# Kernel tuning notes

Hardware: AMD Instinct MI355X
Metric: run time of the kernel (lower is better)

Reference implementation:

```python
import jax, jax.numpy as jnp
import numpy as np

B, S = 256, 500
NQ, DQ, DV, M, F = 10000, 128, 256, 50, 512


def _kaiming(key, shape, fan_in):
    return jax.random.normal(key, shape, dtype=jnp.float32) * np.sqrt(2.0 / fan_in)


def setup_inputs() -> dict:
    key = jax.random.key(0)
    ks = jax.random.split(key, 24)
    inp = {
        'q_data': jax.random.randint(ks[0], (B, S), 0, NQ, dtype=jnp.int32),
        'qa_data': jax.random.randint(ks[1], (B, S), 0, 2 * NQ, dtype=jnp.int32),
        'target': jax.random.randint(ks[2], (B, S), 0, 3, dtype=jnp.int32),
        'time_data': jax.random.randint(ks[3], (B, S), 0, 9902, dtype=jnp.int32),
        'attempt_data': jax.random.randint(ks[4], (B, S), 0, 4000, dtype=jnp.int32),
        'hint_data': jax.random.randint(ks[5], (B, S), 0, 60, dtype=jnp.int32),
        'hintTotal_data': jax.random.randint(ks[6], (B, S), 0, 60, dtype=jnp.int32),
    }
    # embedding tables (padding row 0 zeroed, as in torch padding_idx=0)
    inp['q_emb'] = _kaiming(ks[7], (NQ + 1, DQ), DQ).at[0].set(0.0)
    inp['qa_emb'] = _kaiming(ks[8], (2 * NQ + 1, DV), DV).at[0].set(0.0)
    inp['time_emb'] = _kaiming(ks[9], (9902, DQ), DQ).at[0].set(0.0)
    inp['attempt_emb'] = _kaiming(ks[10], (4000, DQ), DQ).at[0].set(0.0)
    inp['hint_total_emb'] = _kaiming(ks[11], (60, DQ), DQ).at[0].set(0.0)
    # memory init
    inp['Mk'] = _kaiming(ks[12], (M, DQ), DQ)
    inp['Mv0'] = _kaiming(ks[13], (M, DV), DV)
    # difficulty linears (shared weights applied twice)
    inp['diff_W'] = _kaiming(ks[14], (DQ, DQ), DQ)
    inp['diff_b'] = jnp.zeros((DQ,), jnp.float32)
    inp['diff2_W'] = _kaiming(ks[15], (DQ, DQ), DQ)
    inp['diff2_b'] = jnp.zeros((DQ,), jnp.float32)
    # DKVMN write head: erase/add linears (DV -> DV)
    inp['erase_W'] = _kaiming(ks[16], (DV, DV), DV)
    inp['erase_b'] = jnp.zeros((DV,), jnp.float32)
    inp['add_W'] = _kaiming(ks[17], (DV, DV), DV)
    inp['add_b'] = jnp.zeros((DV,), jnp.float32)
    # readout
    inp['read_W'] = _kaiming(ks[18], (F, DV + DQ), DV + DQ)
    inp['read_b'] = jnp.zeros((F,), jnp.float32)
    inp['pred_W'] = _kaiming(ks[19], (1, F), F)
    inp['pred_b'] = jnp.zeros((1,), jnp.float32)
    return inp


def reference(q_data, qa_data, target, time_data, attempt_data, hint_data, hintTotal_data,
              q_emb, qa_emb, time_emb, attempt_emb, hint_total_emb,
              Mk, Mv0, diff_W, diff_b, diff2_W, diff2_b,
              erase_W, erase_b, add_W, add_b, read_W, read_b, pred_W, pred_b):
    lin1 = lambda x: x @ diff_W.T + diff_b
    lin2 = lambda x: x @ diff2_W.T + diff2_b

    qe = q_emb[q_data]                        # [B,S,DQ]
    te = time_emb[time_data]
    ae = attempt_emb[attempt_data]
    he = hint_total_emb[hint_data]            # forward uses hint_total_embed for both
    hte = hint_total_emb[hintTotal_data]

    time_final = jax.nn.sigmoid(lin2(jnp.tanh(lin1(te + qe))))
    diff_final = jax.nn.sigmoid(lin2(jnp.tanh(lin1(hte + he + ae + qe))))
    q_proc = lin1(qe + diff_final * (he + hte + ae))  # [B,S,DQ]
    qa_e = qa_emb[qa_data]                            # [B,S,DV]

    Mv_init = jnp.broadcast_to(Mv0[None], (q_data.shape[0], M, DV))

    def step(Mv, inp):
        q, qa = inp                                   # [B,DQ], [B,DV]
        w = jax.nn.softmax(q @ Mk.T, axis=-1)         # [B,M]
        read = jnp.einsum('bm,bmd->bd', w, Mv)        # [B,DV]
        e = jax.nn.sigmoid(qa @ erase_W.T + erase_b)  # [B,DV]
        a = jnp.tanh(qa @ add_W.T + add_b)            # [B,DV]
        Mv = Mv * (1.0 - w[:, :, None] * e[:, None, :]) + w[:, :, None] * a[:, None, :]
        return Mv, read

    _, reads = jax.lax.scan(step, Mv_init,
                            (jnp.swapaxes(q_proc, 0, 1), jnp.swapaxes(qa_e, 0, 1)))
    reads = jnp.swapaxes(reads, 0, 1)                 # [B,S,DV]

    input_embed = q_proc + time_final * te            # [B,S,DQ]
    predict_input = jnp.concatenate([reads, input_embed], axis=-1)
    rc = jnp.tanh(predict_input @ read_W.T + read_b)  # [B,S,F]
    pred = (rc @ pred_W.T + pred_b).reshape(-1)       # [B*S]

    t1 = target.reshape(-1)
    mask = t1 >= 1
    y = jnp.where(mask, t1 - 1, 0).astype(jnp.float32)
    # BCE with logits: log(1+e^x) - x*y
    lelem = jnp.logaddexp(0.0, pred) - pred * y
    n = jnp.maximum(jnp.sum(mask.astype(jnp.float32)), 1.0)
    loss = jnp.sum(jnp.where(mask, lelem, 0.0)) / n
    maskf = mask.astype(jnp.float32)
    return loss, jax.nn.sigmoid(pred) * maskf, y * maskf
```

## Files before the change

kernel.cpp:

```cpp
#include <hip/hip_runtime.h>
#include <cstdint>
#include <cstddef>

#define NB 256
#define SQ 500
#define NROWS (NB * SQ)
#define DQ 128
#define DV 256
#define MM 50
#define FF 512
#define NQA 20096
#define WSTRIDE 52
#define WT 10

typedef _Float16 half8 __attribute__((ext_vector_type(8)));
typedef float floatx4 __attribute__((ext_vector_type(4)));
typedef float f2 __attribute__((ext_vector_type(2)));
typedef unsigned int u32;
typedef unsigned short u16;

typedef __attribute__((address_space(1))) void gvoid;
typedef __attribute__((address_space(3))) void lvoid;

__device__ __forceinline__ void gl16(const u16* g, u16* l) {
    __builtin_amdgcn_global_load_lds((gvoid*)g, (lvoid*)l, 16, 0, 0);
}

__device__ __forceinline__ float4 ld4(const float* p) {
    return *reinterpret_cast<const float4*>(p);
}
__device__ __forceinline__ float sigf(float x) { return 1.f / (1.f + __expf(-x)); }
__device__ __forceinline__ float tanhfast(float x) { return 2.f / (1.f + __expf(-2.f * x)) - 1.f; }
__device__ __forceinline__ int gmap(int l, int s0, int CS) {
    int b = (unsigned)l / (unsigned)CS;
    return b * SQ + s0 + (l - b * CS);
}
__device__ __forceinline__ void st4h(u16* dst, float4 v) {
    _Float16 h0 = (_Float16)v.x, h1 = (_Float16)v.y, h2 = (_Float16)v.z, h3 = (_Float16)v.w;
    ushort4 u;
    u.x = *(u16*)&h0; u.y = *(u16*)&h1; u.z = *(u16*)&h2; u.w = *(u16*)&h3;
    *(ushort4*)dst = u;
}
__device__ __forceinline__ float h2f(u16 b) { _Float16 h; *(u16*)&h = b; return (float)h; }
__device__ __forceinline__ u16 f2h(float x) { _Float16 h = (_Float16)x; return *(u16*)&h; }

__global__ __launch_bounds__(256) void cvt16(
    const float* __restrict__ s, u16* __restrict__ d, int n4)
{
    int i = blockIdx.x * 256 + threadIdx.x;
    if (i < n4) st4h(d + 4 * (size_t)i, ld4(s + 4 * (size_t)i));
}

__global__ __launch_bounds__(256) void wcvt(
    const float* __restrict__ s0, const float* __restrict__ s1,
    const float* __restrict__ s2, const float* __restrict__ s3,
    const float* __restrict__ s4, u16* __restrict__ dst)
{
    int i = blockIdx.x * 256 + threadIdx.x;
    if (i >= 90112) return;
    const float* s; int off;
    if (i < 4096)       { s = s0; off = 0; }
    else if (i < 8192)  { s = s1; off = 4096; }
    else if (i < 24576) { s = s2; off = 8192; }
    else if (i < 40960) { s = s3; off = 24576; }
    else                { s = s4; off = 40960; }
    st4h(dst + 4 * (size_t)i, ld4(s + 4 * (size_t)(i - off)));
}

__global__ __launch_bounds__(256) void mkcvt(
    const float* __restrict__ Mk, u16* __restrict__ Mkh)
{
    int i = blockIdx.x * 256 + threadIdx.x;
    if (i >= 64 * 32) return;
    int row = i >> 5;
    float4 v = (row < MM) ? ld4(Mk + (size_t)row * DQ + (i & 31) * 4)
                          : float4{0.f, 0.f, 0.f, 0.f};
    st4h(Mkh + 4 * (size_t)i, v);
}

__global__ __launch_bounds__(256) void prep128(
    const int* __restrict__ q_data, const int* __restrict__ time_data,
    const int* __restrict__ attempt_data, const int* __restrict__ hint_data,
    const int* __restrict__ hintT_data,
    const float* __restrict__ q_emb, const float* __restrict__ time_emb,
    const float* __restrict__ attempt_emb, const float* __restrict__ ht_emb,
    u16* __restrict__ Xp, u16* __restrict__ S3p, u16* __restrict__ QEp,
    int s0, int CS, int Nc)
{
    int g = blockIdx.x * 256 + threadIdx.x;
    int l = g >> 5;
    int kq = (g & 31) << 2;
    if (l >= Nc) return;
    int n = gmap(l, s0, CS);
    float4 qe  = ld4(q_emb       + (size_t)q_data[n]       * DQ + kq);
    float4 te  = ld4(time_emb    + (size_t)time_data[n]    * DQ + kq);
    float4 ae  = ld4(attempt_emb + (size_t)attempt_data[n] * DQ + kq);
    float4 he  = ld4(ht_emb      + (size_t)hint_data[n]    * DQ + kq);
    float4 hte = ld4(ht_emb      + (size_t)hintT_data[n]   * DQ + kq);
    size_t off = (size_t)l * DQ + kq;
    float4 x1, s3, x2;
    x1.x = te.x + qe.x; x1.y = te.y + qe.y; x1.z = te.z + qe.z; x1.w = te.w + qe.w;
    s3.x = he.x + hte.x + ae.x; s3.y = he.y + hte.y + ae.y;
    s3.z = he.z + hte.z + ae.z; s3.w = he.w + hte.w + ae.w;
    x2.x = s3.x + qe.x; x2.y = s3.y + qe.y; x2.z = s3.z + qe.z; x2.w = s3.w + qe.w;
    st4h(Xp + off, x1);
    st4h(Xp + (size_t)Nc * DQ + off, x2);
    st4h(S3p + off, s3);
    st4h(QEp + off, qe);
}

__global__ __launch_bounds__(256, 2) void gemm12(
    const u16* __restrict__ A, const u16* __restrict__ W1h,
    const u16* __restrict__ W2h, const float* __restrict__ b1,
    const float* __restrict__ b2, u16* __restrict__ Yh,
    const u16* __restrict__ QEp, const u16* __restrict__ S3p, int Nc)
{
    __shared__ u16 smem[32768];
    u16* At = smem;
    u16* Bt = smem + 8192;
    u16* Tt = smem + 16384;
    const int tid = threadIdx.x;
    const int row0 = blockIdx.x * 128;
    const int lane = tid & 63, wv = tid >> 6;
    const int wr = (wv >> 1) * 64, wc = (wv & 1) * 64;
    const int q = lane >> 4, c0 = lane & 15;

    floatx4 acc[4][4];
#pragma unroll
    for (int m = 0; m < 4; ++m)
#pragma unroll
        for (int n = 0; n < 4; ++n) acc[m][n] = (floatx4)0.f;

    for (int kt = 0; kt < 128; kt += 64) {
#pragma unroll
        for (int j = 0; j < 4; ++j) {
            int f = tid + j * 256; int r = f >> 3; int lg = (f & 7) ^ (r & 7);
            gl16(A + (size_t)(row0 + r) * 128 + kt + lg * 8, &At[f * 8]);
        }
#pragma unroll
        for (int j = 0; j < 4; ++j) {
            int f = tid + j * 256; int r = f >> 3; int lg = (f & 7) ^ (r & 7);
            gl16(W1h + (size_t)r * 128 + kt + lg * 8, &Bt[f * 8]);
        }
        __syncthreads();
#pragma unroll
        for (int kk = 0; kk < 2; ++kk) {
            half8 af[4], bf[4];
#pragma unroll
            for (int m = 0; m < 4; ++m) {
                int row = wr + m * 16 + c0;
                af[m] = *(half8*)&At[row * 64 + ((((kk << 2) | q)) ^ (row & 7)) * 8];
            }
#pragma unroll
            for (int n = 0; n < 4; ++n) {
                int row = wc + n * 16 + c0;
                bf[n] = *(half8*)&Bt[row * 64 + ((((kk << 2) | q)) ^ (row & 7)) * 8];
            }
#pragma unroll
            for (int m = 0; m < 4; ++m)
#pragma unroll
                for (int n = 0; n < 4; ++n)
                    acc[m][n] = __builtin_amdgcn_mfma_f32_16x16x32_f16(af[m], bf[n], acc[m][n], 0, 0, 0);
        }
        __syncthreads();
    }

    {
        float bv1[4];
#pragma unroll
        for (int n = 0; n < 4; ++n) bv1[n] = b1[wc + n * 16 + c0];
#pragma unroll
        for (int m = 0; m < 4; ++m)
#pragma unroll
            for (int r4 = 0; r4 < 4; ++r4) {
                int row = wr + m * 16 + q * 4 + r4;
#pragma unroll
                for (int n = 0; n < 4; ++n) {
                    int col = wc + n * 16 + c0;
                    float v = tanhfast(acc[m][n][r4] + bv1[n]);
                    int tile = col >> 6, cl = col & 63, gl = cl >> 3;
                    Tt[tile * 8192 + row * 64 + ((gl ^ (row & 7)) << 3) + (cl & 7)] = f2h(v);
                }
            }
    }
#pragma unroll
    for (int m = 0; m < 4; ++m)
#pragma unroll
        for (int n = 0; n < 4; ++n) acc[m][n] = (floatx4)0.f;

#pragma unroll
    for (int j = 0; j < 4; ++j) {
        int f = tid + j * 256; int r = f >> 3; int lg = (f & 7) ^ (r & 7);
        gl16(W2h + (size_t)r * 128 + 0 + lg * 8, &Bt[f * 8]);
    }
    __syncthreads();

#pragma unroll
    for (int kt = 0; kt < 2; ++kt) {
#pragma unroll
        for (int kk = 0; kk < 2; ++kk) {
            half8 af[4], bf[4];
#pragma unroll
            for (int m = 0; m < 4; ++m) {
                int row = wr + m * 16 + c0;
                af[m] = *(half8*)&Tt[kt * 8192 + row * 64 + ((((kk << 2) | q)) ^ (row & 7)) * 8];
            }
#pragma unroll
            for (int n = 0; n < 4; ++n) {
                int row = wc + n * 16 + c0;
                bf[n] = *(half8*)&Bt[row * 64 + ((((kk << 2) | q)) ^ (row & 7)) * 8];
            }
#pragma unroll
            for (int m = 0; m < 4; ++m)
#pragma unroll
                for (int n = 0; n < 4; ++n)
                    acc[m][n] = __builtin_amdgcn_mfma_f32_16x16x32_f16(af[m], bf[n], acc[m][n], 0, 0, 0);
        }
        if (kt == 0) {
            __syncthreads();
#pragma unroll
            for (int j = 0; j < 4; ++j) {
                int f = tid + j * 256; int r = f >> 3; int lg = (f & 7) ^ (r & 7);
                gl16(W2h + (size_t)r * 128 + 64 + lg * 8, &Bt[f * 8]);
            }
            __syncthreads();
        }
    }

    float bv[4];
#pragma unroll
    for (int n = 0; n < 4; ++n) bv[n] = b2[wc + n * 16 + c0];
#pragma unroll
    for (int m = 0; m < 4; ++m)
#pragma unroll
        for (int r4 = 0; r4 < 4; ++r4) {
            int row = row0 + wr + m * 16 + q * 4 + r4;
#pragma unroll
            for (int n = 0; n < 4; ++n) {
                int col = wc + n * 16 + c0;
                float v = sigf(acc[m][n][r4] + bv[n]);
                if (row < Nc) {
                    Yh[(size_t)row * 128 + col] = f2h(v);
                } else {
                    size_t o = (size_t)(row - Nc) * 128 + col;
                    float qe = h2f(QEp[o]), s3 = h2f(S3p[o]);
                    Yh[(size_t)row * 128 + col] = f2h(fmaf(v, s3, qe));
                }
            }
        }
}

__global__ __launch_bounds__(256, 2) void gemm3w(
    const u16* __restrict__ X3, const u16* __restrict__ W1h,
    const float* __restrict__ b1, const u16* __restrict__ Mkh,
    const int* __restrict__ tidx, const float* __restrict__ temb,
    const u16* __restrict__ TF, u16* __restrict__ RDIE,
    float* __restrict__ Wb, int s0, int CS)
{
    __shared__ u16 smem[32768];
    u16* At = smem;
    u16* Bt = smem + 8192;
    u16* Tt = smem + 16384;
    const int tid = threadIdx.x;
    const int row0 = blockIdx.x * 128;
    const int lane = tid & 63, wv = tid >> 6;
    const int wr = (wv >> 1) * 64, wc = (wv & 1) * 64;
    const int q = lane >> 4, c0 = lane & 15;

    floatx4 acc[4][4];
#pragma unroll
    for (int m = 0; m < 4; ++m)
#pragma unroll
        for (int n = 0; n < 4; ++n) acc[m][n] = (floatx4)0.f;

    for (int kt = 0; kt < 128; kt += 64) {
#pragma unroll
        for (int j = 0; j < 4; ++j) {
            int f = tid + j * 256; int r = f >> 3; int lg = (f & 7) ^ (r & 7);
            gl16(X3 + (size_t)(row0 + r) * 128 + kt + lg * 8, &At[f * 8]);
        }
#pragma unroll
        for (int j = 0; j < 4; ++j) {
            int f = tid + j * 256; int r = f >> 3; int lg = (f & 7) ^ (r & 7);
            gl16(W1h + (size_t)r * 128 + kt + lg * 8, &Bt[f * 8]);
        }
        __syncthreads();
#pragma unroll
        for (int kk = 0; kk < 2; ++kk) {
            half8 af[4], bf[4];
#pragma unroll
            for (int m = 0; m < 4; ++m) {
                int row = wr + m * 16 + c0;
                af[m] = *(half8*)&At[row * 64 + ((((kk << 2) | q)) ^ (row & 7)) * 8];
            }
#pragma unroll
            for (int n = 0; n < 4; ++n) {
                int row = wc + n * 16 + c0;
                bf[n] = *(half8*)&Bt[row * 64 + ((((kk << 2) | q)) ^ (row & 7)) * 8];
            }
#pragma unroll
            for (int m = 0; m < 4; ++m)
#pragma unroll
                for (int n = 0; n < 4; ++n)
                    acc[m][n] = __builtin_amdgcn_mfma_f32_16x16x32_f16(af[m], bf[n], acc[m][n], 0, 0, 0);
        }
        __syncthreads();
    }

    {
        float bv1[4];
#pragma unroll
        for (int n = 0; n < 4; ++n) bv1[n] = b1[wc + n * 16 + c0];
#pragma unroll
        for (int m = 0; m < 4; ++m)
#pragma unroll
            for (int r4 = 0; r4 < 4; ++r4) {
                int rloc = wr + m * 16 + q * 4 + r4;
                int grow = row0 + rloc;
                int nmap = gmap(grow, s0, CS);
                const float* terow = temb + (size_t)tidx[nmap] * 128;
#pragma unroll
                for (int n = 0; n < 4; ++n) {
                    int col = wc + n * 16 + c0;
                    float qp = acc[m][n][r4] + bv1[n];
                    int tile = col >> 6, cl = col & 63, gl = cl >> 3;
                    Tt[tile * 8192 + rloc * 64 + ((gl ^ (rloc & 7)) << 3) + (cl & 7)] = f2h(qp);
                    float tf = h2f(TF[(size_t)grow * 128 + col]);
                    RDIE[(size_t)grow * 384 + 256 + col] = f2h(fmaf(tf, terow[col], qp));
                }
            }
    }
#pragma unroll
    for (int j = 0; j < 4; ++j) {
        int f = tid + j * 256;
        int fl = f & 511;
        int ktile = f >> 9;
        int r = fl >> 3;
        int lg = (fl & 7) ^ (r & 7);
        gl16(Mkh + (size_t)r * 128 + ktile * 64 + lg * 8, &Bt[f * 8]);
    }
    __syncthreads();

    const int wrW = wv * 32;
    floatx4 acc2[2][4];
#pragma unroll
    for (int m = 0; m < 2; ++m)
#pragma unroll
        for (int n = 0; n < 4; ++n) acc2[m][n] = (floatx4)0.f;
#pragma unroll
    for (int kt = 0; kt < 2; ++kt)
#pragma unroll
        for (int kk = 0; kk < 2; ++kk) {
            half8 af[2], bf[4];
#pragma unroll
            for (int m = 0; m < 2; ++m) {
                int row = wrW + m * 16 + c0;
                af[m] = *(half8*)&Tt[kt * 8192 + row * 64 + ((((kk << 2) | q)) ^ (row & 7)) * 8];
            }
#pragma unroll
            for (int n = 0; n < 4; ++n) {
                int row = n * 16 + c0;
                bf[n] = *(half8*)&Bt[kt * 4096 + row * 64 + ((((kk << 2) | q)) ^ (row & 7)) * 8];
            }
#pragma unroll
            for (int m = 0; m < 2; ++m)
#pragma unroll
                for (int n = 0; n < 4; ++n)
                    acc2[m][n] = __builtin_amdgcn_mfma_f32_16x16x32_f16(af[m], bf[n], acc2[m][n], 0, 0, 0);
        }
    __syncthreads();

    float* Sred = (float*)smem;
#pragma unroll
    for (int m = 0; m < 2; ++m)
#pragma unroll
        for (int r4 = 0; r4 < 4; ++r4) {
            int row = wrW + m * 16 + q * 4 + r4;
#pragma unroll
            for (int n = 0; n < 4; ++n)
                Sred[row * 67 + n * 16 + c0] = acc2[m][n][r4];
        }
    __syncthreads();

    if (tid < 128) {
        float* s = &Sred[tid * 67];
        float mx = -3.0e38f;
#pragma unroll
        for (int m = 0; m < MM; ++m) mx = fmaxf(mx, s[m]);
        float sum = 0.f;
#pragma unroll
        for (int m = 0; m < MM; ++m) { float e = __expf(s[m] - mx); s[m] = e; sum += e; }
        float inv = 1.f / sum;
#pragma unroll
        for (int m = 0; m < MM; ++m) s[m] *= inv;
        s[50] = 0.f; s[51] = 0.f;
    }
    __syncthreads();

    for (int i = tid; i < 128 * 13; i += 256) {
        int row = i / 13, seg = i - row * 13;
        float4 v;
        v.x = Sred[row * 67 + seg * 4 + 0];
        v.y = Sred[row * 67 + seg * 4 + 1];
        v.z = Sred[row * 67 + seg * 4 + 2];
        v.w = Sred[row * 67 + seg * 4 + 3];
        *(float4*)(Wb + (size_t)(row0 + row) * WSTRIDE + seg * 4) = v;
    }
}

template <int MODE>
__global__ __launch_bounds__(256, 2) void gemm16(
    const u16* __restrict__ A, const u16* __restrict__ W0,
    const u16* __restrict__ W1, const float* __restrict__ b0,
    const float* __restrict__ b1, u16* __restrict__ Yh,
    float* __restrict__ Yf,
    u16* __restrict__ AUX, const float* __restrict__ predW,
    int K)
{
    __shared__ u16 smem[2 * 128 * 64];
    u16* At = smem;
    u16* Bt = smem + 128 * 64;
    const int tid = threadIdx.x;
    const int row0 = blockIdx.x * 128;
    const int by = blockIdx.y;

    const u16* Wp;
    int col0;
    if constexpr (MODE == 4) { Wp = (by < 2) ? W0 : W1; col0 = (by & 1) * 128; }
    else { Wp = W0; col0 = by * 128; }
    const float* bias = (MODE == 4 && by >= 2) ? b1 : b0;

    floatx4 acc[4][4];
#pragma unroll
    for (int m = 0; m < 4; ++m)
#pragma unroll
        for (int n = 0; n < 4; ++n) acc[m][n] = (floatx4)0.f;

    const int lane = tid & 63, wv = tid >> 6;
    const int wr = (wv >> 1) * 64, wc = (wv & 1) * 64;
    const int q = lane >> 4, c0 = lane & 15;

    for (int kt = 0; kt < K; kt += 64) {
#pragma unroll
        for (int j = 0; j < 4; ++j) {
            int f = tid + j * 256;
            int r = f >> 3;
            int lg = (f & 7) ^ (r & 7);
            gl16(A + (size_t)(row0 + r) * K + kt + lg * 8, &At[f * 8]);
        }
#pragma unroll
        for (int j = 0; j < 4; ++j) {
            int f = tid + j * 256;
            int r = f >> 3;
            int lg = (f & 7) ^ (r & 7);
            gl16(Wp + (size_t)(col0 + r) * K + kt + lg * 8, &Bt[f * 8]);
        }
        __syncthreads();
#pragma unroll
        for (int kk = 0; kk < 2; ++kk) {
            half8 af[4], bf[4];
#pragma unroll
            for (int m = 0; m < 4; ++m) {
                int row = wr + m * 16 + c0;
                af[m] = *(half8*)&At[row * 64 + ((((kk << 2) | q)) ^ (row & 7)) * 8];
            }
#pragma unroll
            for (int n = 0; n < 4; ++n) {
                int row = wc + n * 16 + c0;
                bf[n] = *(half8*)&Bt[row * 64 + ((((kk << 2) | q)) ^ (row & 7)) * 8];
            }
#pragma unroll
            for (int m = 0; m < 4; ++m)
#pragma unroll
                for (int n = 0; n < 4; ++n)
                    acc[m][n] = __builtin_amdgcn_mfma_f32_16x16x32_f16(af[m], bf[n], acc[m][n], 0, 0, 0);
        }
        __syncthreads();
    }

    float bv[4];
#pragma unroll
    for (int n = 0; n < 4; ++n) bv[n] = bias[col0 + wc + n * 16 + c0];

    if constexpr (MODE == 5) {
        float pw[4];
#pragma unroll
        for (int n = 0; n < 4; ++n) pw[n] = predW[col0 + wc + n * 16 + c0];
        float* red = (float*)smem;
#pragma unroll
        for (int m = 0; m < 4; ++m)
#pragma unroll
            for (int r4 = 0; r4 < 4; ++r4) {
                int row = wr + m * 16 + q * 4 + r4;
                float pp = 0.f;
#pragma unroll
                for (int n = 0; n < 4; ++n)
                    pp = fmaf(tanhfast(acc[m][n][r4] + bv[n]), pw[n], pp);
                red[row * 33 + (wv & 1) * 16 + c0] = pp;
            }
        __syncthreads();
        if (tid < 128) {
            float s = 0.f;
#pragma unroll
            for (int j = 0; j < 32; ++j) s += red[tid * 33 + j];
            atomicAdd(&Yf[row0 + tid], s);
        }
    } else {
#pragma unroll
        for (int m = 0; m < 4; ++m)
#pragma unroll
            for (int r4 = 0; r4 < 4; ++r4) {
                int row = row0 + wr + m * 16 + q * 4 + r4;
#pragma unroll
                for (int n = 0; n < 4; ++n) {
                    int col = col0 + wc + n * 16 + c0;
                    float v = acc[m][n][r4] + bv[n];
                    bool isE = (by < 2);
                    v = isE ? sigf(v) : tanhfast(v);
                    AUX[((size_t)row * 256 + col) * 2 + (isE ? 0 : 1)] = f2h(v);
                }
            }
    }
}

__global__ __launch_bounds__(256, 1) void scan_kernel(
    const float* __restrict__ Wb, const int* __restrict__ qa_data,
    const u32* __restrict__ EAtab,
    const float* __restrict__ Mv0, float* __restrict__ MvSt,
    u16* __restrict__ RDIE, int CS, int s0, int first)
{
    __shared__ float wt[2][WT * WSTRIDE];
    const int b = blockIdx.x;
    const int d = threadIdx.x;

    f2 mv[25];
    if (first) {
#pragma unroll
        for (int j = 0; j < 25; ++j) {
            mv[j].x = Mv0[(2 * j) * DV + d];
            mv[j].y = Mv0[(2 * j + 1) * DV + d];
        }
    } else {
#pragma unroll
        for (int j = 0; j < 25; ++j) {
            mv[j].x = MvSt[((size_t)b * MM + 2 * j) * DV + d];
            mv[j].y = MvSt[((size_t)b * MM + 2 * j + 1) * DV + d];
        }
    }

    const float* wbase = Wb + (size_t)b * CS * WSTRIDE;
    const int* qap = qa_data + (size_t)b * SQ + s0;
    u16* rp = RDIE + (size_t)b * CS * 384 + d;

    const int NT = CS / WT;
    const bool loader = (d < (WT * WSTRIDE / 4));

    if (loader) *(float4*)&wt[0][d * 4] = ld4(wbase + d * 4);
    u32 ea[WT];
    {
        int qi[WT];
#pragma unroll
        for (int i = 0; i < WT; ++i) qi[i] = qap[i];
#pragma unroll
        for (int i = 0; i < WT; ++i) ea[i] = EAtab[(size_t)qi[i] * DV + d];
    }
    __syncthreads();

    int cur = 0;
    for (int tile = 0; tile < NT; ++tile) {
        float4 wreg;
        u32 ean[WT];
        const bool havenext = (tile + 1 < NT);
        if (havenext) {
            if (loader) wreg = ld4(wbase + (size_t)(tile + 1) * WT * WSTRIDE + d * 4);
            int qn[WT];
#pragma unroll
            for (int i = 0; i < WT; ++i) qn[i] = qap[(tile + 1) * WT + i];
#pragma unroll
            for (int i = 0; i < WT; ++i) ean[i] = EAtab[(size_t)qn[i] * DV + d];
        }

        float4 wpp[2][13];
#pragma unroll
        for (int i = 0; i < 13; ++i)
            wpp[0][i] = *(const float4*)&wt[cur][i * 4];

#pragma unroll
        for (int s = 0; s < WT; ++s) {
            if (s + 1 < WT) {
#pragma unroll
                for (int i = 0; i < 13; ++i)
                    wpp[(s + 1) & 1][i] =
                        *(const float4*)&wt[cur][(s + 1) * WSTRIDE + i * 4];
            }
            const f2* w2 = (const f2*)wpp[s & 1];
            u32 eav = ea[s];
            float e = h2f((u16)(eav & 0xffff));
            float a = h2f((u16)(eav >> 16));
            f2 e2; e2.x = e; e2.y = e;
            f2 a2; a2.x = a; a2.y = a;
            f2 r0 = (f2)0.f, r1 = (f2)0.f, r2 = (f2)0.f, r3 = (f2)0.f;
#pragma unroll
            for (int j = 0; j < 24; j += 4) {
                f2 w_0 = w2[j + 0], w_1 = w2[j + 1], w_2 = w2[j + 2], w_3 = w2[j + 3];
                r0 += w_0 * mv[j + 0];
                r1 += w_1 * mv[j + 1];
                r2 += w_2 * mv[j + 2];
                r3 += w_3 * mv[j + 3];
                f2 t0 = a2 - e2 * mv[j + 0];
                f2 t1 = a2 - e2 * mv[j + 1];
                f2 t2 = a2 - e2 * mv[j + 2];
                f2 t3 = a2 - e2 * mv[j + 3];
                mv[j + 0] += w_0 * t0;
                mv[j + 1] += w_1 * t1;
                mv[j + 2] += w_2 * t2;
                mv[j + 3] += w_3 * t3;
            }
            {
                f2 w24 = w2[24];
                r0 += w24 * mv[24];
                f2 t = a2 - e2 * mv[24];
                mv[24] += w24 * t;
            }
            f2 rs = (r0 + r1) + (r2 + r3);
            rp[(size_t)(tile * WT + s) * 384] = f2h(rs.x + rs.y);
        }

        if (havenext) {
            if (loader) *(float4*)&wt[1 - cur][d * 4] = wreg;
#pragma unroll
            for (int i = 0; i < WT; ++i) ea[i] = ean[i];
            __syncthreads();
            cur ^= 1;
        }
    }

#pragma unroll
    for (int j = 0; j < 25; ++j) {
        MvSt[((size_t)b * MM + 2 * j) * DV + d]     = mv[j].x;
        MvSt[((size_t)b * MM + 2 * j + 1) * DV + d] = mv[j].y;
    }
}

__global__ __launch_bounds__(256) void loss_part(
    const float* __restrict__ P, const int* __restrict__ target,
    const float* __restrict__ pred_b, float* __restrict__ out,
    float* __restrict__ R2, int s0, int CS, int Nc)
{
    int l = blockIdx.x * 256 + threadIdx.x;
    float le = 0.f, mf = 0.f;
    if (l < Nc) {
        int n = gmap(l, s0, CS);
        float p = P[l] + pred_b[0];
        int t = target[n];
        float y = (t >= 1) ? (float)(t - 1) : 0.f;
        float sig = 1.f / (1.f + __expf(-p));
        if (t >= 1) {
            mf = 1.f;
            le = fmaxf(p, 0.f) + log1pf(__expf(-fabsf(p))) - p * y;
        }
        out[1 + n] = sig * mf;
        out[1 + NROWS + n] = y * mf;
    }
#pragma unroll
    for (int off = 32; off; off >>= 1) {
        le += __shfl_down(le, off);
        mf += __shfl_down(mf, off);
    }
    __shared__ float sl[4], sm[4];
    int wid = threadIdx.x >> 6;
    if ((threadIdx.x & 63) == 0) { sl[wid] = le; sm[wid] = mf; }
    __syncthreads();
    if (threadIdx.x == 0) {
        atomicAdd(R2, sl[0] + sl[1] + sl[2] + sl[3]);
        atomicAdd(R2 + 1, sm[0] + sm[1] + sm[2] + sm[3]);
    }
}

__global__ void loss_fin(const float* __restrict__ R2, float* __restrict__ out)
{
    out[0] = R2[0] / fmaxf(R2[1], 1.f);
}

extern "C" void kernel_launch(void* const* d_in, const int* in_sizes, int n_in,
                              void* d_out, int out_size, void* d_ws, size_t ws_size,
                              hipStream_t stream)
{
    const int* q_data       = (const int*)d_in[0];
    const int* qa_data      = (const int*)d_in[1];
    const int* target       = (const int*)d_in[2];
    const int* time_data    = (const int*)d_in[3];
    const int* attempt_data = (const int*)d_in[4];
    const int* hint_data    = (const int*)d_in[5];
    const int* hintT_data   = (const int*)d_in[6];
    const float* q_emb    = (const float*)d_in[7];
    const float* qa_emb   = (const float*)d_in[8];
    const float* time_emb = (const float*)d_in[9];
    const float* att_emb  = (const float*)d_in[10];
    const float* ht_emb   = (const float*)d_in[11];
    const float* Mk       = (const float*)d_in[12];
    const float* Mv0      = (const float*)d_in[13];
    const float* diff_W   = (const float*)d_in[14];
    const float* diff_b   = (const float*)d_in[15];
    const float* diff2_W  = (const float*)d_in[16];
    const float* diff2_b  = (const float*)d_in[17];
    const float* erase_W  = (const float*)d_in[18];
    const float* erase_b  = (const float*)d_in[19];
    const float* add_W    = (const float*)d_in[20];
    const float* add_b    = (const float*)d_in[21];
    const float* read_W   = (const float*)d_in[22];
    const float* read_b   = (const float*)d_in[23];
    const float* pred_W   = (const float*)d_in[24];
    const float* pred_b   = (const float*)d_in[25];
    float* out = (float*)d_out;
    (void)in_sizes; (void)n_in; (void)out_size;

    static const int cs_opts[] = {500, 250, 100, 50, 20, 10};
    const size_t FIXED = 44700000ull;
    int CS = 0;
    for (int i = 0; i < 6; ++i) {
        size_t need = (size_t)NB * cs_opts[i] * 2016ull + FIXED;
        if (need <= ws_size) { CS = cs_opts[i]; break; }
    }
    if (CS == 0) return;
    const int NCH = SQ / CS;
    const int Nc = NB * CS;

    float* MvSt  = (float*)d_ws;
    float* wbuf  = MvSt + (size_t)NB * MM * DV;
    float* bufP  = wbuf + (size_t)Nc * WSTRIDE;
    float* bufR2 = bufP + Nc;
    u16*  Xp     = (u16*)(bufR2 + 4);
    u16*  S3p    = Xp + (size_t)2 * Nc * 128;
    u16*  QEp    = S3p + (size_t)Nc * 128;
    u16*  RDIE   = QEp + (size_t)Nc * 128;
    u16*  dWh    = RDIE + (size_t)Nc * 384;
    u16*  d2Wh   = dWh + 16384;
    u16*  eWh    = d2Wh + 16384;
    u16*  aWh    = eWh + 65536;
    u16*  rWh    = aWh + 65536;
    u16*  qaEh   = rWh + 196608;
    u16*  Mkh    = qaEh + 5120256;
    u32*  EAtab  = (u32*)(Mkh + 8192);

    wcvt<<<352, 256, 0, stream>>>(diff_W, diff2_W, erase_W, add_W, read_W, dWh);
    cvt16<<<5001, 256, 0, stream>>>(qa_emb, qaEh, 5120256 / 4);
    mkcvt<<<8, 256, 0, stream>>>(Mk, Mkh);
    hipMemsetAsync(bufR2, 0, 4 * sizeof(float), stream);

    gemm16<4><<<dim3(NQA / 128, 4), 256, 0, stream>>>(
        qaEh, eWh, aWh, erase_b, add_b, nullptr, nullptr,
        (u16*)EAtab, nullptr, 256);

    for (int c = 0; c < NCH; ++c) {
        const int s0 = c * CS;

        prep128<<<Nc / 8, 256, 0, stream>>>(
            q_data, time_data, attempt_data, hint_data, hintT_data,
            q_emb, time_emb, att_emb, ht_emb, Xp, S3p, QEp, s0, CS, Nc);

        gemm12<<<2 * Nc / 128, 256, 0, stream>>>(
            Xp, dWh, d2Wh, diff_b, diff2_b, Xp, QEp, S3p, Nc);

        gemm3w<<<Nc / 128, 256, 0, stream>>>(
            Xp + (size_t)Nc * 128, dWh, diff_b, Mkh,
            time_data, time_emb, Xp, RDIE, wbuf, s0, CS);

        scan_kernel<<<NB, DV, 0, stream>>>(
            wbuf, qa_data, EAtab, Mv0, MvSt, RDIE, CS, s0, c == 0 ? 1 : 0);

        hipMemsetAsync(bufP, 0, (size_t)Nc * sizeof(float), stream);
        gemm16<5><<<dim3(Nc / 128, 4), 256, 0, stream>>>(
            RDIE, rWh, nullptr, read_b, nullptr, nullptr, bufP,
            nullptr, pred_W, 384);

        loss_part<<<Nc / 256, 256, 0, stream>>>(bufP, target, pred_b, out, bufR2, s0, CS, Nc);
    }

    loss_fin<<<1, 1, 0, stream>>>(bufR2, out);
}
```

Before: 645.6 us.

## Swap gemm16 grid axes, raise its occupancy, restructure scan weight registers

gemm16 now puts the column-tile index on blockIdx.x and the row-tile index on blockIdx.y, so the four column tiles that share one A row block run next to each other and can reuse it in cache. Its launch bounds go from 2 to 4 blocks per CU, which pushes the compiler to use fewer registers in exchange for more resident waves. The scan kernel's double-buffered weight arrays become a current/next register pair pinned with empty asm barriers, and the inner loop is written as a single 25-step loop. The register-pinning change is meant to control allocation and avoid spills, but the tighter register budget in gemm16 could cause spills of its own.

Measured after the change: 662.9 us. 1.03x slower.

```diff
diff --git a/kernel.cpp b/kernel.cpp
--- a/kernel.cpp
+++ b/kernel.cpp
@@ -43,6 +43,11 @@
 }
 __device__ __forceinline__ float h2f(u16 b) { _Float16 h; *(u16*)&h = b; return (float)h; }
 __device__ __forceinline__ u16 f2h(float x) { _Float16 h = (_Float16)x; return *(u16*)&h; }
+
+#define KEEP4(v) asm volatile("" : "+v"(v.x), "+v"(v.y), "+v"(v.z), "+v"(v.w))
+#define CBF(arr, k) ((((k) & 3) == 0) ? arr[(k) >> 2].x : \
+                     (((k) & 3) == 1) ? arr[(k) >> 2].y : \
+                     (((k) & 3) == 2) ? arr[(k) >> 2].z : arr[(k) >> 2].w)
 
 __global__ __launch_bounds__(256) void cvt16(
     const float* __restrict__ s, u16* __restrict__ d, int n4)
@@ -409,7 +414,7 @@
 }
 
 template <int MODE>
-__global__ __launch_bounds__(256, 2) void gemm16(
+__global__ __launch_bounds__(256, 4) void gemm16(
     const u16* __restrict__ A, const u16* __restrict__ W0,
     const u16* __restrict__ W1, const float* __restrict__ b0,
     const float* __restrict__ b1, u16* __restrict__ Yh,
@@ -421,8 +426,8 @@
     u16* At = smem;
     u16* Bt = smem + 128 * 64;
     const int tid = threadIdx.x;
-    const int row0 = blockIdx.x * 128;
-    const int by = blockIdx.y;
+    const int row0 = blockIdx.y * 128;
+    const int by = blockIdx.x;
 
     const u16* Wp;
     int col0;
@@ -580,20 +585,19 @@
             for (int i = 0; i < WT; ++i) ean[i] = EAtab[(size_t)qn[i] * DV + d];
         }
 
-        float4 wpp[2][13];
-#pragma unroll
-        for (int i = 0; i < 13; ++i)
-            wpp[0][i] = *(const float4*)&wt[cur][i * 4];
+        float4 cb[13], nb[13];
+#pragma unroll
+        for (int i = 0; i < 13; ++i) cb[i] = *(const float4*)&wt[cur][i * 4];
+#pragma unroll
+        for (int i = 0; i < 13; ++i) KEEP4(cb[i]);
 
 #pragma unroll
         for (int s = 0; s < WT; ++s) {
             if (s + 1 < WT) {
 #pragma unroll
                 for (int i = 0; i < 13; ++i)
-                    wpp[(s + 1) & 1][i] =
-                        *(const float4*)&wt[cur][(s + 1) * WSTRIDE + i * 4];
-            }
-            const f2* w2 = (const f2*)wpp[s & 1];
+                    nb[i] = *(const float4*)&wt[cur][(s + 1) * WSTRIDE + i * 4];
+            }
             u32 eav = ea[s];
             float e = h2f((u16)(eav & 0xffff));
             float a = h2f((u16)(eav >> 16));
@@ -601,29 +605,25 @@
             f2 a2; a2.x = a; a2.y = a;
             f2 r0 = (f2)0.f, r1 = (f2)0.f, r2 = (f2)0.f, r3 = (f2)0.f;
 #pragma unroll
-            for (int j = 0; j < 24; j += 4) {
-                f2 w_0 = w2[j + 0], w_1 = w2[j + 1], w_2 = w2[j + 2], w_3 = w2[j + 3];
-                r0 += w_0 * mv[j + 0];
-                r1 += w_1 * mv[j + 1];
-                r2 += w_2 * mv[j + 2];
-                r3 += w_3 * mv[j + 3];
-                f2 t0 = a2 - e2 * mv[j + 0];
-                f2 t1 = a2 - e2 * mv[j + 1];
-                f2 t2 = a2 - e2 * mv[j + 2];
-                f2 t3 = a2 - e2 * mv[j + 3];
-                mv[j + 0] += w_0 * t0;
-                mv[j + 1] += w_1 * t1;
-                mv[j + 2] += w_2 * t2;
-                mv[j + 3] += w_3 * t3;
-            }
-            {
-                f2 w24 = w2[24];
-                r0 += w24 * mv[24];
-                f2 t = a2 - e2 * mv[24];
-                mv[24] += w24 * t;
+            for (int j = 0; j < 25; ++j) {
+                f2 w2;
+                w2.x = CBF(cb, 2 * j);
+                w2.y = CBF(cb, 2 * j + 1);
+                if ((j & 3) == 0)      r0 += w2 * mv[j];
+                else if ((j & 3) == 1) r1 += w2 * mv[j];
+                else if ((j & 3) == 2) r2 += w2 * mv[j];
+                else                   r3 += w2 * mv[j];
+                f2 tt = a2 - e2 * mv[j];
+                mv[j] += w2 * tt;
             }
             f2 rs = (r0 + r1) + (r2 + r3);
             rp[(size_t)(tile * WT + s) * 384] = f2h(rs.x + rs.y);
+            if (s + 1 < WT) {
+#pragma unroll
+                for (int i = 0; i < 13; ++i) KEEP4(nb[i]);
+#pragma unroll
+                for (int i = 0; i < 13; ++i) cb[i] = nb[i];
+            }
         }
 
         if (havenext) {
@@ -748,7 +748,7 @@
     mkcvt<<<8, 256, 0, stream>>>(Mk, Mkh);
     hipMemsetAsync(bufR2, 0, 4 * sizeof(float), stream);
 
-    gemm16<4><<<dim3(NQA / 128, 4), 256, 0, stream>>>(
+    gemm16<4><<<dim3(4, NQA / 128), 256, 0, stream>>>(
         qaEh, eWh, aWh, erase_b, add_b, nullptr, nullptr,
         (u16*)EAtab, nullptr, 256);
 
@@ -770,7 +770,7 @@
             wbuf, qa_data, EAtab, Mv0, MvSt, RDIE, CS, s0, c == 0 ? 1 : 0);
 
         hipMemsetAsync(bufP, 0, (size_t)Nc * sizeof(float), stream);
-        gemm16<5><<<dim3(Nc / 128, 4), 256, 0, stream>>>(
+        gemm16<5><<<dim3(4, Nc / 128), 256, 0, stream>>>(
             RDIE, rWh, nullptr, read_b, nullptr, nullptr, bufP,
             nullptr, pred_W, 384);
 
```

## Store QE/S3 inside RDIE, drop atomics, swap grid axes, raise gemm16 occupancy

Applied to the files above, without the earlier changes.

prep128 now writes the qe and s3 embeddings straight into RDIE rows (stride 384), so the separate QEp/S3p buffers are no longer needed. gemm12 reads them from there. gemm16 swaps its grid axes so the four column blocks of the same rows run next to each other. The read/pred GEMM writes four per-column-block partial sums, which removes the atomicAdd and the memset, and loss_part sums them. Launch bounds move to 4 blocks per CU, which may limit registers and cause spills. The smaller workspace need per row may also allow a larger chunk size.

Measured after the change: 610.5 us. 5.4% less time.

```diff
diff --git a/kernel.cpp b/kernel.cpp
--- a/kernel.cpp
+++ b/kernel.cpp
@@ -84,7 +84,7 @@
     const int* __restrict__ hintT_data,
     const float* __restrict__ q_emb, const float* __restrict__ time_emb,
     const float* __restrict__ attempt_emb, const float* __restrict__ ht_emb,
-    u16* __restrict__ Xp, u16* __restrict__ S3p, u16* __restrict__ QEp,
+    u16* __restrict__ Xp, u16* __restrict__ RDIE,
     int s0, int CS, int Nc)
 {
     int g = blockIdx.x * 256 + threadIdx.x;
@@ -105,15 +105,15 @@
     x2.x = s3.x + qe.x; x2.y = s3.y + qe.y; x2.z = s3.z + qe.z; x2.w = s3.w + qe.w;
     st4h(Xp + off, x1);
     st4h(Xp + (size_t)Nc * DQ + off, x2);
-    st4h(S3p + off, s3);
-    st4h(QEp + off, qe);
+    st4h(RDIE + (size_t)l * 384 + kq, qe);
+    st4h(RDIE + (size_t)l * 384 + 128 + kq, s3);
 }
 
 __global__ __launch_bounds__(256, 2) void gemm12(
     const u16* __restrict__ A, const u16* __restrict__ W1h,
     const u16* __restrict__ W2h, const float* __restrict__ b1,
     const float* __restrict__ b2, u16* __restrict__ Yh,
-    const u16* __restrict__ QEp, const u16* __restrict__ S3p, int Nc)
+    const u16* __restrict__ RDIE, int Nc)
 {
     __shared__ u16 smem[32768];
     u16* At = smem;
@@ -242,8 +242,8 @@
                 if (row < Nc) {
                     Yh[(size_t)row * 128 + col] = f2h(v);
                 } else {
-                    size_t o = (size_t)(row - Nc) * 128 + col;
-                    float qe = h2f(QEp[o]), s3 = h2f(S3p[o]);
+                    size_t o = (size_t)(row - Nc) * 384 + col;
+                    float qe = h2f(RDIE[o]), s3 = h2f(RDIE[o + 128]);
                     Yh[(size_t)row * 128 + col] = f2h(fmaf(v, s3, qe));
                 }
             }
@@ -409,7 +409,7 @@
 }
 
 template <int MODE>
-__global__ __launch_bounds__(256, 2) void gemm16(
+__global__ __launch_bounds__(256, 4) void gemm16(
     const u16* __restrict__ A, const u16* __restrict__ W0,
     const u16* __restrict__ W1, const float* __restrict__ b0,
     const float* __restrict__ b1, u16* __restrict__ Yh,
@@ -421,8 +421,8 @@
     u16* At = smem;
     u16* Bt = smem + 128 * 64;
     const int tid = threadIdx.x;
-    const int row0 = blockIdx.x * 128;
-    const int by = blockIdx.y;
+    const int row0 = blockIdx.y * 128;
+    const int by = blockIdx.x;
 
     const u16* Wp;
     int col0;
@@ -503,7 +503,7 @@
             float s = 0.f;
 #pragma unroll
             for (int j = 0; j < 32; ++j) s += red[tid * 33 + j];
-            atomicAdd(&Yf[row0 + tid], s);
+            Yf[(size_t)(row0 + tid) * 4 + by] = s;
         }
     } else {
 #pragma unroll
@@ -643,7 +643,7 @@
 }
 
 __global__ __launch_bounds__(256) void loss_part(
-    const float* __restrict__ P, const int* __restrict__ target,
+    const float* __restrict__ P4, const int* __restrict__ target,
     const float* __restrict__ pred_b, float* __restrict__ out,
     float* __restrict__ R2, int s0, int CS, int Nc)
 {
@@ -651,7 +651,8 @@
     float le = 0.f, mf = 0.f;
     if (l < Nc) {
         int n = gmap(l, s0, CS);
-        float p = P[l] + pred_b[0];
+        float4 p4 = ld4(P4 + (size_t)l * 4);
+        float p = (p4.x + p4.y) + (p4.z + p4.w) + pred_b[0];
         int t = target[n];
         float y = (t >= 1) ? (float)(t - 1) : 0.f;
         float sig = 1.f / (1.f + __expf(-p));
@@ -716,10 +717,10 @@
     (void)in_sizes; (void)n_in; (void)out_size;
 
     static const int cs_opts[] = {500, 250, 100, 50, 20, 10};
-    const size_t FIXED = 44700000ull;
+    const size_t FIXED = 44800000ull;
     int CS = 0;
     for (int i = 0; i < 6; ++i) {
-        size_t need = (size_t)NB * cs_opts[i] * 2016ull + FIXED;
+        size_t need = (size_t)NB * cs_opts[i] * 1504ull + FIXED;
         if (need <= ws_size) { CS = cs_opts[i]; break; }
     }
     if (CS == 0) return;
@@ -728,12 +729,10 @@
 
     float* MvSt  = (float*)d_ws;
     float* wbuf  = MvSt + (size_t)NB * MM * DV;
-    float* bufP  = wbuf + (size_t)Nc * WSTRIDE;
-    float* bufR2 = bufP + Nc;
+    float* bufP4 = wbuf + (size_t)Nc * WSTRIDE;
+    float* bufR2 = bufP4 + (size_t)Nc * 4;
     u16*  Xp     = (u16*)(bufR2 + 4);
-    u16*  S3p    = Xp + (size_t)2 * Nc * 128;
-    u16*  QEp    = S3p + (size_t)Nc * 128;
-    u16*  RDIE   = QEp + (size_t)Nc * 128;
+    u16*  RDIE   = Xp + (size_t)2 * Nc * 128;
     u16*  dWh    = RDIE + (size_t)Nc * 384;
     u16*  d2Wh   = dWh + 16384;
     u16*  eWh    = d2Wh + 16384;
@@ -748,7 +747,7 @@
     mkcvt<<<8, 256, 0, stream>>>(Mk, Mkh);
     hipMemsetAsync(bufR2, 0, 4 * sizeof(float), stream);
 
-    gemm16<4><<<dim3(NQA / 128, 4), 256, 0, stream>>>(
+    gemm16<4><<<dim3(4, NQA / 128), 256, 0, stream>>>(
         qaEh, eWh, aWh, erase_b, add_b, nullptr, nullptr,
         (u16*)EAtab, nullptr, 256);
 
@@ -757,10 +756,10 @@
 
         prep128<<<Nc / 8, 256, 0, stream>>>(
             q_data, time_data, attempt_data, hint_data, hintT_data,
-            q_emb, time_emb, att_emb, ht_emb, Xp, S3p, QEp, s0, CS, Nc);
+            q_emb, time_emb, att_emb, ht_emb, Xp, RDIE, s0, CS, Nc);
 
         gemm12<<<2 * Nc / 128, 256, 0, stream>>>(
-            Xp, dWh, d2Wh, diff_b, diff2_b, Xp, QEp, S3p, Nc);
+            Xp, dWh, d2Wh, diff_b, diff2_b, Xp, RDIE, Nc);
 
         gemm3w<<<Nc / 128, 256, 0, stream>>>(
             Xp + (size_t)Nc * 128, dWh, diff_b, Mkh,
@@ -769,12 +768,11 @@
         scan_kernel<<<NB, DV, 0, stream>>>(
             wbuf, qa_data, EAtab, Mv0, MvSt, RDIE, CS, s0, c == 0 ? 1 : 0);
 
-        hipMemsetAsync(bufP, 0, (size_t)Nc * sizeof(float), stream);
-        gemm16<5><<<dim3(Nc / 128, 4), 256, 0, stream>>>(
-            RDIE, rWh, nullptr, read_b, nullptr, nullptr, bufP,
+        gemm16<5><<<dim3(4, Nc / 128), 256, 0, stream>>>(
+            RDIE, rWh, nullptr, read_b, nullptr, nullptr, bufP4,
             nullptr, pred_W, 384);
 
-        loss_part<<<Nc / 256, 256, 0, stream>>>(bufP, target, pred_b, out, bufR2, s0, CS, Nc);
+        loss_part<<<Nc / 256, 256, 0, stream>>>(bufP4, target, pred_b, out, bufR2, s0, CS, Nc);
     }
 
     loss_fin<<<1, 1, 0, stream>>>(bufR2, out);
```
